# Optimization experiments

Hardware: AMD Instinct MI355X
Metric: run time of the kernel (lower is better)

## Reference

```python
import jax, jax.numpy as jnp
import numpy as np

B, N, C_Q, H, C_HID = 1, 2048, 256, 8, 32


def setup_inputs() -> dict:
    key = jax.random.key(0)
    ks = jax.random.split(key, 8)
    s_in = 1.0 / np.sqrt(C_Q)
    s_hid = 1.0 / np.sqrt(H * C_HID)
    return {
        "q_x": jax.random.normal(ks[0], (B, N, C_Q), jnp.float32),
        "kv_x": jax.random.normal(ks[1], (B, N, C_Q), jnp.float32),
        "attn_bias": jax.random.normal(ks[2], (B, H, N, N), jnp.float32),
        "Wq": jax.random.normal(ks[3], (C_Q, H * C_HID), jnp.float32) * s_in,
        "Wk": jax.random.normal(ks[4], (C_Q, H * C_HID), jnp.float32) * s_in,
        "Wv": jax.random.normal(ks[5], (C_Q, H * C_HID), jnp.float32) * s_in,
        "Wg": jax.random.normal(ks[6], (C_Q, H * C_HID), jnp.float32) * s_in,
        "Wo": jax.random.normal(ks[7], (H * C_HID, C_Q), jnp.float32) * s_hid,
    }


def reference(q_x, kv_x, attn_bias, Wq, Wk, Wv, Wg, Wo):
    # QKV projections (no bias), split heads: [B, H, N, C_hid]
    def proj(x, W):
        y = x @ W  # [B, N, H*C_hid]
        return y.reshape(y.shape[:-1] + (H, C_HID)).swapaxes(-2, -3)

    scale = 1.0 / np.sqrt(C_HID)
    q = proj(q_x, Wq) * scale
    k = proj(kv_x, Wk)
    v = proj(kv_x, Wv)

    # scores + external additive bias, stable softmax
    scores = jnp.einsum("bhqc,bhkc->bhqk", q, k) + attn_bias
    a = jax.nn.softmax(scores, axis=-1)
    o = jnp.einsum("bhqk,bhkc->bhqc", a, v)  # [B, H, N, C_hid]

    o = o.swapaxes(-2, -3)  # [B, N, H, C_hid]
    # sigmoid gating from query input
    g = jax.nn.sigmoid(q_x @ Wg).reshape(o.shape)
    o = o * g
    o = o.reshape(o.shape[:-2] + (H * C_HID,))
    return o @ Wo  # [B, N, C_q]
```

## Files before the change

### kernel.cpp

```cpp
#include <hip/hip_runtime.h>
#include <hip/hip_bf16.h>
#include <stdint.h>

typedef __attribute__((ext_vector_type(8))) short short8;
typedef __attribute__((ext_vector_type(8))) __bf16 bf16x8;
typedef __attribute__((ext_vector_type(4))) float f32x4;
typedef __attribute__((ext_vector_type(4))) float float4v;
typedef __attribute__((ext_vector_type(4))) unsigned short us4;
typedef unsigned int u32;
typedef __attribute__((address_space(3))) u32 lds_u32;
typedef const __attribute__((address_space(1))) u32 g_u32;

#define NSEQ 2048
#define L2E 1.44269504088896f

static __device__ __forceinline__ unsigned short f2bf(float x){
  union { float f; u32 u; } v; v.f = x;
  u32 r = v.u + 0x7fffu + ((v.u >> 16) & 1u);
  return (unsigned short)(r >> 16);
}
static __device__ __forceinline__ float bf2f(unsigned short s){
  union { float f; u32 u; } v; v.u = ((u32)s) << 16; return v.f;
}
static __device__ __forceinline__ void gload16(const void* g, void* l){
  __builtin_amdgcn_global_load_lds((g_u32*)g, (lds_u32*)l, 16, 0, 0);
}
static __device__ __forceinline__ f32x4 mfma16(bf16x8 a, bf16x8 b, f32x4 c){
  return __builtin_amdgcn_mfma_f32_16x16x32_bf16(a, b, c, 0, 0, 0);
}
static __device__ __forceinline__ bf16x8 ldfrag(const void* p){
  return *(const bf16x8*)p;
}
#define MEMFENCE() asm volatile("" ::: "memory")

__global__ __launch_bounds__(256) void cvt_kernel(const float* __restrict__ qx,
                           const float* __restrict__ kvx,
                           const float* __restrict__ Wq, const float* __restrict__ Wk,
                           const float* __restrict__ Wv, const float* __restrict__ Wg,
                           const float* __restrict__ Wo,
                           unsigned short* __restrict__ Xbq, unsigned short* __restrict__ Xbkv,
                           unsigned short* __restrict__ Wt4, unsigned short* __restrict__ Wot){
  __shared__ float T[64][65];
  int bid = blockIdx.x;
  if (bid < 512){
    int i4 = (bid*256 + threadIdx.x) * 4;
    float4v q = *(const float4v*)(qx + i4);
    float4v k = *(const float4v*)(kvx + i4);
    us4 qo, ko;
    #pragma unroll
    for (int j = 0; j < 4; ++j){ qo[j] = f2bf(q[j]); ko[j] = f2bf(k[j]); }
    *(us4*)(Xbq + i4) = qo;
    *(us4*)(Xbkv + i4) = ko;
  } else {
    int b2 = bid - 512;
    int w = b2 >> 4, tile = b2 & 15, tr = tile >> 2, tc = tile & 3;
    const float* W = (w==0)?Wq:((w==1)?Wk:((w==2)?Wv:((w==3)?Wg:Wo)));
    int t = threadIdx.x;
    int rl = t >> 4, cq = t & 15;
    #pragma unroll
    for (int p = 0; p < 4; ++p){
      int r = p*16 + rl;
      float4v v = *(const float4v*)(W + (size_t)(tr*64 + r)*256 + tc*64 + cq*4);
      #pragma unroll
      for (int j = 0; j < 4; ++j) T[r][cq*4+j] = v[j];
    }
    __syncthreads();
    float s = (w==0) ? 0.17677669529663687f : 1.f;
    #pragma unroll
    for (int p = 0; p < 4; ++p){
      int o = p*16 + rl;
      us4 pk;
      #pragma unroll
      for (int j = 0; j < 4; ++j) pk[j] = f2bf(T[cq*4+j][o] * s);
      int og = tc*64 + o, ig = tr*64 + cq*4;
      if (w < 4) *(us4*)(Wt4 + (size_t)w*65536 + og*256 + ig) = pk;
      else       *(us4*)(Wot + (size_t)og*256 + ig) = pk;
    }
  }
}

__global__ __launch_bounds__(256) void proj_kernel(const unsigned short* __restrict__ Xbq,
     const unsigned short* __restrict__ Xbkv, const unsigned short* __restrict__ Wt4,
     unsigned short* __restrict__ Qb, unsigned short* __restrict__ Kb,
     unsigned short* __restrict__ Vt, unsigned short* __restrict__ Gg){
  __shared__ unsigned short Asm[64*256];
  __shared__ unsigned short Bsm[64*256];
  int mt = blockIdx.x;
  int nt = blockIdx.y;
  int col0 = nt * 64;
  int w = col0 >> 8;
  const unsigned short* A = (w==0 || w==3) ? Xbq : Xbkv;
  int tid = threadIdx.x, lane = tid & 63, wid = tid >> 6;
  const char* Ab = (const char*)A   + (size_t)mt*64*512;
  const char* Bb = (const char*)Wt4 + (size_t)col0*512;
  char* Asl = (char*)Asm; char* Bsl = (char*)Bsm;
  #pragma unroll
  for (int it = 0; it < 8; ++it){
    int o = it*4096 + wid*1024 + lane*16;
    int row = o >> 9, b = o & 511;
    int sb = (o & ~511) + (b ^ ((row & 15) << 4));
    gload16(Ab + sb, Asl + it*4096 + wid*1024);
    gload16(Bb + sb, Bsl + it*4096 + wid*1024);
  }
  __syncthreads();
  int ml = lane & 15, kg = lane >> 4;
  int m = wid*16 + ml;
  bf16x8 afr[8];
  #pragma unroll
  for (int ks = 0; ks < 8; ++ks)
    afr[ks] = ldfrag(Asl + m*512 + ((ks*64 + kg*16) ^ (ml << 4)));
  f32x4 acc[4];
  #pragma unroll
  for (int ct = 0; ct < 4; ++ct){
    acc[ct] = (f32x4){0.f,0.f,0.f,0.f};
    int oo = ct*16 + ml;
    #pragma unroll
    for (int ks = 0; ks < 8; ++ks){
      bf16x8 bfr = ldfrag(Bsl + oo*512 + ((ks*64 + kg*16) ^ (ml << 4)));
      acc[ct] = mfma16(afr[ks], bfr, acc[ct]);
    }
  }
  #pragma unroll
  for (int ct = 0; ct < 4; ++ct){
    int colg = col0 + ct*16 + ml;
    int cw = colg & 255, hh = cw >> 5, c = cw & 31;
    int n0 = mt*64 + wid*16 + kg*4;
    if (w == 2){
      us4 pk;
      pk[0]=f2bf(acc[ct][0]); pk[1]=f2bf(acc[ct][1]);
      pk[2]=f2bf(acc[ct][2]); pk[3]=f2bf(acc[ct][3]);
      *(us4*)((char*)Vt + ((size_t)(hh*32 + c)*NSEQ + n0)*2) = pk;
    } else {
      #pragma unroll
      for (int r = 0; r < 4; ++r){
        int n = n0 + r;
        float v = acc[ct][r];
        if (w == 0)      Qb[((size_t)hh*NSEQ + n)*32 + c] = f2bf(v);
        else if (w == 1) Kb[((size_t)hh*NSEQ + n)*32 + c] = f2bf(v);
        else             Gg[(size_t)n*256 + cw] = f2bf(1.f/(1.f + __expf(-v)));
      }
    }
  }
}

__global__ __launch_bounds__(256, 4) void attn_kernel(const unsigned short* __restrict__ Qb,
    const unsigned short* __restrict__ Kb, const unsigned short* __restrict__ Vt,
    const float* __restrict__ bias,
    float* __restrict__ Opart, float* __restrict__ Mpart, float* __restrict__ Lpart){
  __shared__ unsigned short Ksm[4][2048];
  __shared__ unsigned short Vsm[4][2048];
  __shared__ unsigned short Psm[4096];
  int bid = blockIdx.x;
  int h = bid >> 7, qt = (bid >> 2) & 31, ch = bid & 3;
  int q0 = qt * 64;
  int tid = threadIdx.x, lane = tid & 63, wid = tid >> 6;
  int ml = lane & 15, kg = lane >> 4;
  int qw = q0 + wid*16;
  bf16x8 qfr = ldfrag((const char*)Qb + (((size_t)h*NSEQ + qw + ml)*32 + kg*8)*2);
  const char* Kbase = (const char*)Kb + (size_t)h*NSEQ*32*2;
  const char* Vbase = (const char*)Vt + (size_t)h*32*NSEQ*2;
  const float* bias_l = bias + (size_t)h*NSEQ*NSEQ + (size_t)(qw + kg*4)*NSEQ + ch*512 + ml;
  float mreg[4] = {-3e38f,-3e38f,-3e38f,-3e38f};
  float lreg[4] = {0.f,0.f,0.f,0.f};
  f32x4 oacc[2];
  oacc[0] = (f32x4){0.f,0.f,0.f,0.f};
  oacc[1] = (f32x4){0.f,0.f,0.f,0.f};

  auto stage = [&](int t, int buf){
    int tg = ch*8 + t;
    int o = tid*16;
    int n = o >> 6, kb = o & 63;
    gload16(Kbase + (size_t)tg*4096 + (o & ~63) + (kb ^ (((n>>1)&3) << 4)),
            (char*)&Ksm[buf][0] + o);
    int c = o >> 7, vb = o & 127;
    gload16(Vbase + (size_t)c*4096 + (size_t)tg*128 + (vb ^ ((c&7) << 4)),
            (char*)&Vsm[buf][0] + o);
  };

  stage(0, 0);
  stage(1, 1);
  for (int t = 0; t < 8; ++t){
    int cur = t & 3;
    if (t == 7) asm volatile("s_waitcnt vmcnt(0)" ::: "memory");
    else        asm volatile("s_waitcnt vmcnt(2)" ::: "memory");
    __builtin_amdgcn_s_barrier();
    MEMFENCE();
    if (t < 6) stage(t+2, (t+2) & 3);
    float bb[4][4];
    #pragma unroll
    for (int ct = 0; ct < 4; ++ct){
      #pragma unroll
      for (int r = 0; r < 4; ++r)
        bb[ct][r] = bias_l[(size_t)r*NSEQ + t*64 + ct*16];
    }
    f32x4 s[4];
    #pragma unroll
    for (int ct = 0; ct < 4; ++ct){
      f32x4 b;
      #pragma unroll
      for (int r = 0; r < 4; ++r) b[r] = bb[ct][r];
      int n = ct*16 + ml;
      bf16x8 kfr = ldfrag((char*)&Ksm[cur][0] + n*64 + ((kg*16) ^ (((n>>1)&3) << 4)));
      s[ct] = mfma16(qfr, kfr, b);
    }
    float mx[4];
    #pragma unroll
    for (int r = 0; r < 4; ++r){
      mx[r] = fmaxf(fmaxf(s[0][r], s[1][r]), fmaxf(s[2][r], s[3][r]));
    }
    #pragma unroll
    for (int d = 1; d < 16; d <<= 1){
      #pragma unroll
      for (int r = 0; r < 4; ++r) mx[r] = fmaxf(mx[r], __shfl_xor(mx[r], d));
    }
    float sc[4], rs[4];
    #pragma unroll
    for (int r = 0; r < 4; ++r){
      float mn = fmaxf(mreg[r], mx[r]);
      sc[r] = exp2f((mreg[r] - mn) * L2E);
      mreg[r] = mn;
      rs[r] = 0.f;
    }
    #pragma unroll
    for (int ct = 0; ct < 4; ++ct){
      #pragma unroll
      for (int r = 0; r < 4; ++r){
        float pv = exp2f((s[ct][r] - mreg[r]) * L2E);
        s[ct][r] = pv;
        rs[r] += pv;
      }
    }
    #pragma unroll
    for (int d = 1; d < 16; d <<= 1){
      #pragma unroll
      for (int r = 0; r < 4; ++r) rs[r] += __shfl_xor(rs[r], d);
    }
    #pragma unroll
    for (int r = 0; r < 4; ++r) lreg[r] = lreg[r]*sc[r] + rs[r];
    #pragma unroll
    for (int c2 = 0; c2 < 2; ++c2){
      #pragma unroll
      for (int r = 0; r < 4; ++r) oacc[c2][r] *= sc[r];
    }
    #pragma unroll
    for (int ct = 0; ct < 4; ++ct){
      #pragma unroll
      for (int r = 0; r < 4; ++r){
        int q = wid*16 + kg*4 + r;
        int k = ct*16 + ml;
        *(unsigned short*)((char*)Psm + q*128 + ((k*2) ^ ((q&7) << 4))) = f2bf(s[ct][r]);
      }
    }
    int qq = wid*16 + ml;
    #pragma unroll
    for (int ks = 0; ks < 2; ++ks){
      bf16x8 pfr = ldfrag((char*)Psm + qq*128 + ((ks*64 + kg*16) ^ ((qq&7) << 4)));
      #pragma unroll
      for (int c2 = 0; c2 < 2; ++c2){
        int c = c2*16 + ml;
        bf16x8 vfr = ldfrag((char*)&Vsm[cur][0] + c*128 + ((ks*64 + kg*16) ^ ((c&7) << 4)));
        oacc[c2] = mfma16(pfr, vfr, oacc[c2]);
      }
    }
    MEMFENCE();
  }
  size_t pbase = ((size_t)(ch*8 + h)*NSEQ);
  #pragma unroll
  for (int c2 = 0; c2 < 2; ++c2){
    #pragma unroll
    for (int r = 0; r < 4; ++r){
      int q = qw + kg*4 + r;
      Opart[(pbase + q)*32 + c2*16 + ml] = oacc[c2][r];
    }
  }
  if (ml == 0){
    #pragma unroll
    for (int r = 0; r < 4; ++r){
      int q = qw + kg*4 + r;
      Mpart[pbase + q] = mreg[r];
      Lpart[pbase + q] = lreg[r];
    }
  }
}

__global__ __launch_bounds__(256) void combine_kernel(const float* __restrict__ Opart,
    const float* __restrict__ Mpart, const float* __restrict__ Lpart,
    const unsigned short* __restrict__ Gg, unsigned short* __restrict__ Og){
  int n = blockIdx.x*8 + (threadIdx.x >> 5);
  int c = threadIdx.x & 31;
  #pragma unroll
  for (int h = 0; h < 8; ++h){
    float m0 = Mpart[(size_t)(0*8+h)*NSEQ + n], m1 = Mpart[(size_t)(1*8+h)*NSEQ + n];
    float m2 = Mpart[(size_t)(2*8+h)*NSEQ + n], m3 = Mpart[(size_t)(3*8+h)*NSEQ + n];
    float M = fmaxf(fmaxf(m0, m1), fmaxf(m2, m3));
    float e0 = exp2f((m0-M)*L2E), e1 = exp2f((m1-M)*L2E);
    float e2 = exp2f((m2-M)*L2E), e3 = exp2f((m3-M)*L2E);
    float L = Lpart[(size_t)(0*8+h)*NSEQ + n]*e0 + Lpart[(size_t)(1*8+h)*NSEQ + n]*e1
            + Lpart[(size_t)(2*8+h)*NSEQ + n]*e2 + Lpart[(size_t)(3*8+h)*NSEQ + n]*e3;
    float o = Opart[((size_t)(0*8+h)*NSEQ + n)*32 + c]*e0
            + Opart[((size_t)(1*8+h)*NSEQ + n)*32 + c]*e1
            + Opart[((size_t)(2*8+h)*NSEQ + n)*32 + c]*e2
            + Opart[((size_t)(3*8+h)*NSEQ + n)*32 + c]*e3;
    float g = bf2f(Gg[(size_t)n*256 + h*32 + c]);
    Og[(size_t)n*256 + h*32 + c] = f2bf(o / L * g);
  }
}

__global__ __launch_bounds__(256) void oproj_kernel(const unsigned short* __restrict__ Og,
    const unsigned short* __restrict__ Wot, float* __restrict__ out){
  __shared__ unsigned short Asm[64*256];
  __shared__ unsigned short Bsm[64*256];
  int mt = blockIdx.x, nt = blockIdx.y;
  int col0 = nt * 64;
  int tid = threadIdx.x, lane = tid & 63, wid = tid >> 6;
  const char* Ab = (const char*)Og  + (size_t)mt*64*512;
  const char* Bb = (const char*)Wot + (size_t)col0*512;
  char* Asl = (char*)Asm; char* Bsl = (char*)Bsm;
  #pragma unroll
  for (int it = 0; it < 8; ++it){
    int o = it*4096 + wid*1024 + lane*16;
    int row = o >> 9, b = o & 511;
    int sb = (o & ~511) + (b ^ ((row & 15) << 4));
    gload16(Ab + sb, Asl + it*4096 + wid*1024);
    gload16(Bb + sb, Bsl + it*4096 + wid*1024);
  }
  __syncthreads();
  int ml = lane & 15, kg = lane >> 4;
  int m = wid*16 + ml;
  bf16x8 afr[8];
  #pragma unroll
  for (int ks = 0; ks < 8; ++ks)
    afr[ks] = ldfrag(Asl + m*512 + ((ks*64 + kg*16) ^ (ml << 4)));
  f32x4 acc[4];
  #pragma unroll
  for (int ct = 0; ct < 4; ++ct){
    acc[ct] = (f32x4){0.f,0.f,0.f,0.f};
    int oo = ct*16 + ml;
    #pragma unroll
    for (int ks = 0; ks < 8; ++ks){
      bf16x8 bfr = ldfrag(Bsl + oo*512 + ((ks*64 + kg*16) ^ (ml << 4)));
      acc[ct] = mfma16(afr[ks], bfr, acc[ct]);
    }
  }
  #pragma unroll
  for (int ct = 0; ct < 4; ++ct){
    #pragma unroll
    for (int r = 0; r < 4; ++r){
      int mm = mt*64 + wid*16 + kg*4 + r;
      out[(size_t)mm*256 + col0 + ct*16 + ml] = acc[ct][r];
    }
  }
}

extern "C" void kernel_launch(void* const* d_in, const int* in_sizes, int n_in,
                              void* d_out, int out_size, void* d_ws, size_t ws_size,
                              hipStream_t stream) {
  const float* qx   = (const float*)d_in[0];
  const float* kvx  = (const float*)d_in[1];
  const float* bias = (const float*)d_in[2];
  const float* Wq   = (const float*)d_in[3];
  const float* Wk   = (const float*)d_in[4];
  const float* Wv   = (const float*)d_in[5];
  const float* Wg   = (const float*)d_in[6];
  const float* Wo   = (const float*)d_in[7];
  float* out = (float*)d_out;
  char* ws = (char*)d_ws;
  unsigned short* Xbq  = (unsigned short*)(ws);
  unsigned short* Xbkv = (unsigned short*)(ws + (1<<20));
  unsigned short* Wt4  = (unsigned short*)(ws + (2<<20));
  unsigned short* Wot  = (unsigned short*)(ws + (2<<20) + (512<<10));
  unsigned short* Qb   = (unsigned short*)(ws + (3<<20));
  unsigned short* Kb   = (unsigned short*)(ws + (4<<20));
  unsigned short* Vt   = (unsigned short*)(ws + (5<<20));
  unsigned short* Gg   = (unsigned short*)(ws + (6<<20));
  unsigned short* Og   = (unsigned short*)(ws + (7<<20));
  float*          Opart= (float*)(ws + (8<<20));
  float*          Mpart= (float*)(ws + (16<<20));
  float*          Lpart= (float*)(ws + (17<<20));

  cvt_kernel<<<592, 256, 0, stream>>>(qx, kvx, Wq, Wk, Wv, Wg, Wo, Xbq, Xbkv, Wt4, Wot);
  dim3 gp(32, 16);
  proj_kernel<<<gp, 256, 0, stream>>>(Xbq, Xbkv, Wt4, Qb, Kb, Vt, Gg);
  attn_kernel<<<1024, 256, 0, stream>>>(Qb, Kb, Vt, bias, Opart, Mpart, Lpart);
  combine_kernel<<<256, 256, 0, stream>>>(Opart, Mpart, Lpart, Gg, Og);
  dim3 go(32, 4);
  oproj_kernel<<<go, 256, 0, stream>>>(Og, Wot, out);
}
```

Before: 56.68 us.

## Transpose score MFMA so each lane owns a query row, vectorize bias and P stores

```diff
diff --git a/kernel.cpp b/kernel.cpp
--- a/kernel.cpp
+++ b/kernel.cpp
@@ -8,6 +8,7 @@
 typedef __attribute__((ext_vector_type(4))) float float4v;
 typedef __attribute__((ext_vector_type(4))) unsigned short us4;
 typedef unsigned int u32;
+typedef __attribute__((ext_vector_type(2))) u32 u32x2;
 typedef __attribute__((address_space(3))) u32 lds_u32;
 typedef const __attribute__((address_space(1))) u32 g_u32;
 
@@ -21,6 +22,9 @@
 }
 static __device__ __forceinline__ float bf2f(unsigned short s){
   union { float f; u32 u; } v; v.u = ((u32)s) << 16; return v.f;
+}
+static __device__ __forceinline__ u32 cvtpk(float lo, float hi){
+  u32 r; asm("v_cvt_pk_bf16_f32 %0, %1, %2" : "=v"(r) : "v"(lo), "v"(hi)); return r;
 }
 static __device__ __forceinline__ void gload16(const void* g, void* l){
   __builtin_amdgcn_global_load_lds((g_u32*)g, (lds_u32*)l, 16, 0, 0);
@@ -143,7 +147,7 @@
   }
 }
 
-__global__ __launch_bounds__(256, 4) void attn_kernel(const unsigned short* __restrict__ Qb,
+__global__ __launch_bounds__(256) void attn_kernel(const unsigned short* __restrict__ Qb,
     const unsigned short* __restrict__ Kb, const unsigned short* __restrict__ Vt,
     const float* __restrict__ bias,
     float* __restrict__ Opart, float* __restrict__ Mpart, float* __restrict__ Lpart){
@@ -159,9 +163,9 @@
   bf16x8 qfr = ldfrag((const char*)Qb + (((size_t)h*NSEQ + qw + ml)*32 + kg*8)*2);
   const char* Kbase = (const char*)Kb + (size_t)h*NSEQ*32*2;
   const char* Vbase = (const char*)Vt + (size_t)h*32*NSEQ*2;
-  const float* bias_l = bias + (size_t)h*NSEQ*NSEQ + (size_t)(qw + kg*4)*NSEQ + ch*512 + ml;
-  float mreg[4] = {-3e38f,-3e38f,-3e38f,-3e38f};
-  float lreg[4] = {0.f,0.f,0.f,0.f};
+  const float* bias_q = bias + (size_t)h*NSEQ*NSEQ + (size_t)(qw + ml)*NSEQ + ch*512 + kg*4;
+  float mreg = -3e38f;
+  float lreg = 0.f;
   f32x4 oacc[2];
   oacc[0] = (f32x4){0.f,0.f,0.f,0.f};
   oacc[1] = (f32x4){0.f,0.f,0.f,0.f};
@@ -177,84 +181,81 @@
             (char*)&Vsm[buf][0] + o);
   };
 
+  float4v bb[4];
+  #pragma unroll
+  for (int ct = 0; ct < 4; ++ct) bb[ct] = *(const float4v*)(bias_q + ct*16);
+  MEMFENCE();
   stage(0, 0);
   stage(1, 1);
+  int qrow = wid*16 + ml;
+  char* Pb = (char*)Psm + qrow*128;
+  int qs = (ml & 7) << 4;
   for (int t = 0; t < 8; ++t){
     int cur = t & 3;
     if (t == 7) asm volatile("s_waitcnt vmcnt(0)" ::: "memory");
     else        asm volatile("s_waitcnt vmcnt(2)" ::: "memory");
     __builtin_amdgcn_s_barrier();
     MEMFENCE();
-    if (t < 6) stage(t+2, (t+2) & 3);
-    float bb[4][4];
+    f32x4 s[4];
     #pragma unroll
     for (int ct = 0; ct < 4; ++ct){
-      #pragma unroll
-      for (int r = 0; r < 4; ++r)
-        bb[ct][r] = bias_l[(size_t)r*NSEQ + t*64 + ct*16];
-    }
-    f32x4 s[4];
-    #pragma unroll
-    for (int ct = 0; ct < 4; ++ct){
-      f32x4 b;
-      #pragma unroll
-      for (int r = 0; r < 4; ++r) b[r] = bb[ct][r];
       int n = ct*16 + ml;
       bf16x8 kfr = ldfrag((char*)&Ksm[cur][0] + n*64 + ((kg*16) ^ (((n>>1)&3) << 4)));
-      s[ct] = mfma16(qfr, kfr, b);
-    }
-    float mx[4];
-    #pragma unroll
-    for (int r = 0; r < 4; ++r){
-      mx[r] = fmaxf(fmaxf(s[0][r], s[1][r]), fmaxf(s[2][r], s[3][r]));
-    }
-    #pragma unroll
-    for (int d = 1; d < 16; d <<= 1){
-      #pragma unroll
-      for (int r = 0; r < 4; ++r) mx[r] = fmaxf(mx[r], __shfl_xor(mx[r], d));
-    }
-    float sc[4], rs[4];
-    #pragma unroll
-    for (int r = 0; r < 4; ++r){
-      float mn = fmaxf(mreg[r], mx[r]);
-      sc[r] = exp2f((mreg[r] - mn) * L2E);
-      mreg[r] = mn;
-      rs[r] = 0.f;
-    }
+      f32x4 b;
+      #pragma unroll
+      for (int r = 0; r < 4; ++r) b[r] = bb[ct][r];
+      s[ct] = mfma16(kfr, qfr, b);
+    }
+    MEMFENCE();
+    if (t < 7){
+      #pragma unroll
+      for (int ct = 0; ct < 4; ++ct)
+        bb[ct] = *(const float4v*)(bias_q + (t+1)*64 + ct*16);
+    }
+    MEMFENCE();
+    if (t < 6) stage(t+2, (t+2) & 3);
+    MEMFENCE();
+    float m0 = fmaxf(fmaxf(s[0][0],s[0][1]), fmaxf(s[0][2],s[0][3]));
+    float m1 = fmaxf(fmaxf(s[1][0],s[1][1]), fmaxf(s[1][2],s[1][3]));
+    float m2 = fmaxf(fmaxf(s[2][0],s[2][1]), fmaxf(s[2][2],s[2][3]));
+    float m3 = fmaxf(fmaxf(s[3][0],s[3][1]), fmaxf(s[3][2],s[3][3]));
+    float mx = fmaxf(fmaxf(m0,m1), fmaxf(m2,m3));
+    mx = fmaxf(mx, __shfl_xor(mx, 16));
+    mx = fmaxf(mx, __shfl_xor(mx, 32));
+    float mn = fmaxf(mreg, mx);
+    float sc = exp2f((mreg - mn) * L2E);
+    mreg = mn;
+    float rs = 0.f;
     #pragma unroll
     for (int ct = 0; ct < 4; ++ct){
       #pragma unroll
       for (int r = 0; r < 4; ++r){
-        float pv = exp2f((s[ct][r] - mreg[r]) * L2E);
+        float pv = exp2f((s[ct][r] - mn) * L2E);
         s[ct][r] = pv;
-        rs[r] += pv;
+        rs += pv;
       }
     }
-    #pragma unroll
-    for (int d = 1; d < 16; d <<= 1){
-      #pragma unroll
-      for (int r = 0; r < 4; ++r) rs[r] += __shfl_xor(rs[r], d);
-    }
-    #pragma unroll
-    for (int r = 0; r < 4; ++r) lreg[r] = lreg[r]*sc[r] + rs[r];
+    rs += __shfl_xor(rs, 16);
+    rs += __shfl_xor(rs, 32);
+    lreg = lreg*sc + rs;
+    float scq[4];
+    #pragma unroll
+    for (int r = 0; r < 4; ++r) scq[r] = __shfl(sc, kg*4 + r);
     #pragma unroll
     for (int c2 = 0; c2 < 2; ++c2){
       #pragma unroll
-      for (int r = 0; r < 4; ++r) oacc[c2][r] *= sc[r];
+      for (int r = 0; r < 4; ++r) oacc[c2][r] *= scq[r];
     }
     #pragma unroll
     for (int ct = 0; ct < 4; ++ct){
-      #pragma unroll
-      for (int r = 0; r < 4; ++r){
-        int q = wid*16 + kg*4 + r;
-        int k = ct*16 + ml;
-        *(unsigned short*)((char*)Psm + q*128 + ((k*2) ^ ((q&7) << 4))) = f2bf(s[ct][r]);
-      }
-    }
-    int qq = wid*16 + ml;
+      u32x2 pk;
+      pk[0] = cvtpk(s[ct][0], s[ct][1]);
+      pk[1] = cvtpk(s[ct][2], s[ct][3]);
+      *(u32x2*)(Pb + ((ct*32 + kg*8) ^ qs)) = pk;
+    }
     #pragma unroll
     for (int ks = 0; ks < 2; ++ks){
-      bf16x8 pfr = ldfrag((char*)Psm + qq*128 + ((ks*64 + kg*16) ^ ((qq&7) << 4)));
+      bf16x8 pfr = ldfrag(Pb + ((ks*64 + kg*16) ^ qs));
       #pragma unroll
       for (int c2 = 0; c2 < 2; ++c2){
         int c = c2*16 + ml;
@@ -265,20 +266,16 @@
     MEMFENCE();
   }
   size_t pbase = ((size_t)(ch*8 + h)*NSEQ);
+  if (kg == 0){
+    Mpart[pbase + qw + ml] = mreg;
+    Lpart[pbase + qw + ml] = lreg;
+  }
   #pragma unroll
   for (int c2 = 0; c2 < 2; ++c2){
     #pragma unroll
     for (int r = 0; r < 4; ++r){
       int q = qw + kg*4 + r;
       Opart[(pbase + q)*32 + c2*16 + ml] = oacc[c2][r];
-    }
-  }
-  if (ml == 0){
-    #pragma unroll
-    for (int r = 0; r < 4; ++r){
-      int q = qw + kg*4 + r;
-      Mpart[pbase + q] = mreg[r];
-      Lpart[pbase + q] = lreg[r];
     }
   }
 }
```

New measurement: 50.82 us. 1.12x faster.
